# Kernel tuning notes

Hardware: AMD Instinct MI355X
Metric: run time of the kernel (lower is better)

The kernel has to match this reference:

```python
import jax, jax.numpy as jnp
import numpy as np

N_REC_STEPS = 50      # fixed-point iterations for geodesic reconstruction
BN_EPS = 1e-3         # keras BatchNormalization default epsilon


def _dilation2d(x, k):
    # tf.nn.dilation2d, SAME padding: out[p,q] = max_{i,j} x[p+i-1,q+j-1] + k[i,j]
    kk = k[:, :, 0, 0]
    H, W = x.shape[1], x.shape[2]
    xp = jnp.pad(x, ((0, 0), (1, 1), (1, 1), (0, 0)), constant_values=-np.inf)
    vals = [xp[:, i:i + H, j:j + W, :] + kk[i, j] for i in range(3) for j in range(3)]
    return jnp.max(jnp.stack(vals, axis=0), axis=0)


def _erosion2d(x, k):
    # tf.nn.erosion2d (kernel mirrored): out[p,q] = min_{i,j} x[p+i-1,q+j-1] - k[-i,-j]
    kk = k[::-1, ::-1, 0, 0]
    H, W = x.shape[1], x.shape[2]
    xp = jnp.pad(x, ((0, 0), (1, 1), (1, 1), (0, 0)), constant_values=np.inf)
    vals = [xp[:, i:i + H, j:j + W, :] - kk[i, j] for i in range(3) for j in range(3)]
    return jnp.min(jnp.stack(vals, axis=0), axis=0)


def _conv_relu(x, w, b):
    y = jax.lax.conv_general_dilated(x, w, (1, 1), 'VALID',
                                     dimension_numbers=('NHWC', 'HWIO', 'NHWC'))
    return jax.nn.relu(y + b)


def _bn(x, g, b, m, v):
    return g * (x - m) * jax.lax.rsqrt(v + BN_EPS) + b


def _maxpool2(x):
    return jax.lax.reduce_window(x, -np.inf, jax.lax.max,
                                 (1, 2, 2, 1), (1, 2, 2, 1), 'VALID')


def _dilate3_same(x):
    # flat 3x3 structuring element (skimage square(3)) geodesic dilation step
    return jax.lax.reduce_window(x, -np.inf, jax.lax.max,
                                 (1, 3, 3, 1), (1, 1, 1, 1), 'SAME')


def _h_maxima(h, mask):
    # reconstruction-by-dilation of (mask - h) under mask
    marker = mask - h
    def step(m, _):
        m = jnp.minimum(_dilate3_same(m), mask)
        return m, None
    rec, _ = jax.lax.scan(step, marker, None, length=N_REC_STEPS)
    return rec


def setup_inputs() -> dict:
    key = jax.random.key(0)
    ks = jax.random.split(key, 8)
    B, H, W = 32, 256, 256
    inp = {
        'x': jax.random.uniform(ks[0], (B, H, W, 1), dtype=jnp.float32),
        'kernel_open': jnp.zeros((3, 3, 1, 1), jnp.float32),   # flat SE (zero-init)
        'kernel_close': jnp.zeros((3, 3, 1, 1), jnp.float32),
        'conv1_w': 0.1 * jax.random.normal(ks[1], (3, 3, 1, 8), jnp.float32),
        'conv1_b': jnp.zeros((8,), jnp.float32),
        'conv2_w': 0.1 * jax.random.normal(ks[2], (3, 3, 8, 16), jnp.float32),
        'conv2_b': jnp.zeros((16,), jnp.float32),
        'conv3_w': 0.1 * jax.random.normal(ks[3], (3, 3, 16, 32), jnp.float32),
        'conv3_b': jnp.zeros((32,), jnp.float32),
        'conv4_w': 0.1 * jax.random.normal(ks[4], (3, 3, 32, 32), jnp.float32),
        'conv4_b': jnp.zeros((32,), jnp.float32),
        'bn1_g': jnp.ones((8,), jnp.float32), 'bn1_b': jnp.zeros((8,), jnp.float32),
        'bn1_m': jnp.zeros((8,), jnp.float32), 'bn1_v': jnp.ones((8,), jnp.float32),
        'bn2_g': jnp.ones((16,), jnp.float32), 'bn2_b': jnp.zeros((16,), jnp.float32),
        'bn2_m': jnp.zeros((16,), jnp.float32), 'bn2_v': jnp.ones((16,), jnp.float32),
        'bn3_g': jnp.ones((32,), jnp.float32), 'bn3_b': jnp.zeros((32,), jnp.float32),
        'bn3_m': jnp.zeros((32,), jnp.float32), 'bn3_v': jnp.ones((32,), jnp.float32),
        'dense_w': 0.05 * jax.random.uniform(ks[5], (32, 1), dtype=jnp.float32),  # NonNeg
        'dense_b': jnp.zeros((1,), jnp.float32),
    }
    return inp


def reference(x, kernel_open, kernel_close,
              conv1_w, conv1_b, conv2_w, conv2_b, conv3_w, conv3_b, conv4_w, conv4_b,
              bn1_g, bn1_b, bn1_m, bn1_v,
              bn2_g, bn2_b, bn2_m, bn2_v,
              bn3_g, bn3_b, bn3_m, bn3_v,
              dense_w, dense_b):
    # Opening2D then Closing2D (morphological pre-filter)
    xo = _dilation2d(_erosion2d(x, kernel_open), kernel_open)
    xc = _erosion2d(_dilation2d(xo, kernel_close), kernel_close)
    y = _conv_relu(xc, conv1_w, conv1_b)                 # (B,254,254,8)
    y = _bn(y, bn1_g, bn1_b, bn1_m, bn1_v)
    y = _conv_relu(y, conv2_w, conv2_b)                  # (B,252,252,16)
    y = _maxpool2(y)                                     # (B,126,126,16)
    y = _bn(y, bn2_g, bn2_b, bn2_m, bn2_v)
    y = _conv_relu(y, conv3_w, conv3_b)                  # (B,124,124,32)
    y = _bn(y, bn3_g, bn3_b, bn3_m, bn3_v)
    y = _conv_relu(y, conv4_w, conv4_b)                  # (B,122,122,32)
    y = _maxpool2(y)                                     # (B,61,61,32)
    y = jnp.max(y, axis=(1, 2))                          # GlobalMaxPooling2D -> (B,32)
    h = y @ dense_w + dense_b                            # (B,1)
    h = h[:, :, None, None]                              # (B,1,1,1)
    # h-maxima transform: reconstruction by dilation of (xc - h) under xc
    out = _h_maxima(h, xc)                               # (B,256,256,1)
    return (out, h)
```

## Files before the change

kernel.cpp:

```cpp
#include <hip/hip_runtime.h>


#define B_ 32
#define H_ 256
#define W_ 256

__device__ __forceinline__ float4 ld4(const float* p){ return *reinterpret_cast<const float4*>(p); }
__device__ __forceinline__ void st4(float* p, float4 v){ *reinterpret_cast<float4*>(p) = v; }
__device__ __forceinline__ void st4s(float* p, float4 v){ *reinterpret_cast<float4*>(p) = v; }

template<int IS_MAX>
__global__ void morph_k(const float* __restrict__ in, float* __restrict__ out,
                        const float* __restrict__ k9)
{
    int t = blockIdx.x * blockDim.x + threadIdx.x;
    int xq = t & 63; int y = (t >> 6) & 255; int b = t >> 14;
    if (b >= B_) return;
    const float INF = __builtin_inff();
    const float* img = in + (size_t)b * (H_ * W_);
    int x0 = xq * 4;
    float res[4];
    #pragma unroll
    for (int j = 0; j < 4; ++j) res[j] = IS_MAX ? -INF : INF;
    #pragma unroll
    for (int di = -1; di <= 1; ++di) {
        int yy = y + di;
        if (yy < 0 || yy >= H_) continue;
        const float* row = img + yy * W_;
        float w[6];
        w[0] = (x0 > 0) ? row[x0 - 1] : (IS_MAX ? -INF : INF);
        float4 m = ld4(row + x0);
        w[1] = m.x; w[2] = m.y; w[3] = m.z; w[4] = m.w;
        w[5] = (x0 + 4 < W_) ? row[x0 + 4] : (IS_MAX ? -INF : INF);
        #pragma unroll
        for (int dj = -1; dj <= 1; ++dj) {
            float kv = IS_MAX ? k9[(di + 1) * 3 + (dj + 1)]
                              : k9[(1 - di) * 3 + (1 - dj)];
            #pragma unroll
            for (int j = 0; j < 4; ++j) {
                float v = IS_MAX ? (w[j + 1 + dj] + kv) : (w[j + 1 + dj] - kv);
                res[j] = IS_MAX ? fmaxf(res[j], v) : fminf(res[j], v);
            }
        }
    }
    st4(out + (size_t)b * (H_ * W_) + y * W_ + x0,
        make_float4(res[0], res[1], res[2], res[3]));
}

__global__ void conv1_k(const float* __restrict__ xc, float* __restrict__ y1,
                        const float* __restrict__ w, const float* __restrict__ bias,
                        const float* __restrict__ g, const float* __restrict__ bb,
                        const float* __restrict__ mn, const float* __restrict__ vr)
{
    const int S = 254;
    int t = blockIdx.x * blockDim.x + threadIdx.x;
    int total = B_ * S * S;
    if (t >= total) return;
    int x = t % S; int y = (t / S) % S; int b = t / (S * S);
    const float* img = xc + (size_t)b * H_ * W_;
    float acc[8];
    #pragma unroll
    for (int c = 0; c < 8; ++c) acc[c] = bias[c];
    #pragma unroll
    for (int ky = 0; ky < 3; ++ky) {
        #pragma unroll
        for (int kx = 0; kx < 3; ++kx) {
            float iv = img[(y + ky) * W_ + (x + kx)];
            const float* wp = w + (ky * 3 + kx) * 8;
            #pragma unroll
            for (int c = 0; c < 8; ++c) acc[c] = fmaf(iv, wp[c], acc[c]);
        }
    }
    float* op = y1 + (size_t)t * 8;
    #pragma unroll
    for (int c = 0; c < 8; ++c) {
        float z = fmaxf(acc[c], 0.f);
        float s = g[c] / sqrtf(vr[c] + 1.0e-3f);
        op[c] = fmaf(s, z, bb[c] - mn[c] * s);
    }
}

#define C2_PITCH (34 * 34 + 2)
__global__ void __launch_bounds__(256) conv2t_k(
    const float* __restrict__ y1, float* __restrict__ y2,
    const float* __restrict__ w, const float* __restrict__ bias,
    const float* __restrict__ g, const float* __restrict__ bb,
    const float* __restrict__ mn, const float* __restrict__ vr)
{
    const int SIN = 254, POUT = 126;
    __shared__ float lds[8 * C2_PITCH];
    int blk = blockIdx.x;
    int b = blk >> 6; int tt = blk & 63; int ty = tt >> 3, tx = tt & 7;
    int cy0 = ty * 32, cx0 = tx * 32;
    int tid = threadIdx.x;
    const float* in_b = y1 + (size_t)b * SIN * SIN * 8;

    for (int i = tid; i < 34 * 34; i += 256) {
        int r = i / 34, c = i - r * 34;
        int gy = min(cy0 + r, SIN - 1), gx = min(cx0 + c, SIN - 1);
        const float* p = in_b + ((size_t)gy * SIN + gx) * 8;
        float4 a = ld4(p), d = ld4(p + 4);
        lds[0 * C2_PITCH + i] = a.x; lds[1 * C2_PITCH + i] = a.y;
        lds[2 * C2_PITCH + i] = a.z; lds[3 * C2_PITCH + i] = a.w;
        lds[4 * C2_PITCH + i] = d.x; lds[5 * C2_PITCH + i] = d.y;
        lds[6 * C2_PITCH + i] = d.z; lds[7 * C2_PITCH + i] = d.w;
    }
    __syncthreads();

    int lty = tid >> 4, ltx = tid & 15;
    float acc[4][16];
    #pragma unroll
    for (int pos = 0; pos < 4; ++pos)
        #pragma unroll
        for (int c = 0; c < 16; ++c) acc[pos][c] = bias[c];

    #pragma unroll 1
    for (int tap = 0; tap < 9; ++tap) {
        int ky = tap / 3, kx = tap - ky * 3;
        const float* wp = w + tap * 8 * 16;
        #pragma unroll
        for (int pos = 0; pos < 4; ++pos) {
            int pix = (2 * lty + (pos >> 1) + ky) * 34 + (2 * ltx + (pos & 1) + kx);
            float in8[8];
            #pragma unroll
            for (int ci = 0; ci < 8; ++ci) in8[ci] = lds[ci * C2_PITCH + pix];
            #pragma unroll
            for (int ci = 0; ci < 8; ++ci)
                #pragma unroll
                for (int co = 0; co < 16; ++co)
                    acc[pos][co] = fmaf(in8[ci], wp[ci * 16 + co], acc[pos][co]);
        }
    }

    int py = ty * 16 + lty, px = tx * 16 + ltx;
    if (py < POUT && px < POUT) {
        float* op = y2 + ((size_t)b * POUT * POUT + (size_t)py * POUT + px) * 16;
        #pragma unroll
        for (int co = 0; co < 16; ++co) {
            float bst = fmaxf(fmaxf(fmaxf(acc[0][co], 0.f), fmaxf(acc[1][co], 0.f)),
                              fmaxf(fmaxf(acc[2][co], 0.f), fmaxf(acc[3][co], 0.f)));
            float s = g[co] / sqrtf(vr[co] + 1.0e-3f);
            op[co] = fmaf(s, bst, bb[co] - mn[co] * s);
        }
    }
}

template<int CIN, int NCH, int CHP, int SIN>
__device__ __forceinline__ void conv_tile_chunked(
    const float* __restrict__ in_b, const float* __restrict__ w,
    const float* __restrict__ bias, float* lds,
    int y0, int x0, int lty, int ltx, int tid, float acc[32])
{
    const int CHUNK = CIN / NCH, CHQ = CHUNK / 4;
    #pragma unroll
    for (int c = 0; c < 32; ++c) acc[c] = bias[c];
    #pragma unroll 1
    for (int ch = 0; ch < NCH; ++ch) {
        int ci0 = ch * CHUNK;
        if (ch) __syncthreads();
        const int TOT = 18 * 18 * CHQ;
        for (int i = tid; i < TOT; i += 256) {
            int pix = i / CHQ, q = i - pix * CHQ;
            int r = pix / 18, c = pix - r * 18;
            int gy = min(y0 + r, SIN - 1), gx = min(x0 + c, SIN - 1);
            float4 v = ld4(in_b + ((size_t)gy * SIN + gx) * CIN + ci0 + q * 4);
            st4s(lds + (r * 18 + c) * CHP + q * 4, v);
        }
        __syncthreads();
        const float* wb = w + ci0 * 32;
        #pragma unroll 1
        for (int tap = 0; tap < 9; ++tap) {
            int ky = tap / 3, kx = tap - ky * 3;
            const float* lp = lds + ((lty + ky) * 18 + (ltx + kx)) * CHP;
            float v[CHUNK];
            #pragma unroll
            for (int q = 0; q < CHQ; ++q) {
                float4 t4 = *reinterpret_cast<const float4*>(lp + q * 4);
                v[q * 4 + 0] = t4.x; v[q * 4 + 1] = t4.y;
                v[q * 4 + 2] = t4.z; v[q * 4 + 3] = t4.w;
            }
            const float* wt = wb + tap * CIN * 32;
            #pragma unroll
            for (int ci = 0; ci < CHUNK; ++ci)
                #pragma unroll
                for (int co = 0; co < 32; ++co)
                    acc[co] = fmaf(v[ci], wt[ci * 32 + co], acc[co]);
        }
    }
}

__global__ void __launch_bounds__(256) conv3t_k(
    const float* __restrict__ y2, float* __restrict__ y3,
    const float* __restrict__ w, const float* __restrict__ bias,
    const float* __restrict__ g, const float* __restrict__ bb,
    const float* __restrict__ mn, const float* __restrict__ vr)
{
    const int SIN = 126, SOUT = 124;
    __shared__ float lds[18 * 18 * 20];
    int blk = blockIdx.x;
    int b = blk >> 6; int tt = blk & 63; int ty = tt >> 3, tx = tt & 7;
    int tid = threadIdx.x, lty = tid >> 4, ltx = tid & 15;
    float acc[32];
    conv_tile_chunked<16, 1, 20, 126>(y2 + (size_t)b * SIN * SIN * 16, w, bias,
                                      lds, ty * 16, tx * 16, lty, ltx, tid, acc);
    int oy = ty * 16 + lty, ox = tx * 16 + ltx;
    if (oy < SOUT && ox < SOUT) {
        float* op = y3 + ((size_t)b * SOUT * SOUT + (size_t)oy * SOUT + ox) * 32;
        #pragma unroll
        for (int c = 0; c < 32; ++c) {
            float z = fmaxf(acc[c], 0.f);
            float s = g[c] / sqrtf(vr[c] + 1.0e-3f);
            op[c] = fmaf(s, z, bb[c] - mn[c] * s);
        }
    }
}

__global__ void __launch_bounds__(256) conv4t_k(
    const float* __restrict__ y3, float* __restrict__ maxbuf,
    const float* __restrict__ w, const float* __restrict__ bias)
{
    const int SIN = 124, SOUT = 122;
    __shared__ float lds[18 * 18 * 20];
    __shared__ float red[4 * 32];
    int blk = blockIdx.x;
    int b = blk >> 6; int tt = blk & 63; int ty = tt >> 3, tx = tt & 7;
    int tid = threadIdx.x, lty = tid >> 4, ltx = tid & 15;
    float acc[32];
    conv_tile_chunked<32, 2, 20, 124>(y3 + (size_t)b * SIN * SIN * 32, w, bias,
                                      lds, ty * 16, tx * 16, lty, ltx, tid, acc);
    int oy = ty * 16 + lty, ox = tx * 16 + ltx;
    bool valid = (oy < SOUT) && (ox < SOUT);
    #pragma unroll
    for (int c = 0; c < 32; ++c)
        acc[c] = valid ? fmaxf(acc[c], 0.f) : 0.f;
    int lane = tid & 63, wid = tid >> 6;
    #pragma unroll 1
    for (int c = 0; c < 32; ++c) {
        float v = acc[c];
        #pragma unroll
        for (int off = 32; off >= 1; off >>= 1)
            v = fmaxf(v, __shfl_xor(v, off, 64));
        if (lane == 0) red[wid * 32 + c] = v;
    }
    __syncthreads();
    if (tid < 32) {
        int c = tid;
        float mx = fmaxf(fmaxf(red[0 * 32 + c], red[1 * 32 + c]),
                         fmaxf(red[2 * 32 + c], red[3 * 32 + c]));
        atomicMax(reinterpret_cast<int*>(maxbuf) + b * 32 + c, __float_as_int(mx));
    }
}

__global__ void dense_k(const float* __restrict__ maxbuf, const float* __restrict__ dw,
                        const float* __restrict__ db, float* __restrict__ hbuf,
                        float* __restrict__ out_h)
{
    int t = threadIdx.x;
    if (t < B_) {
        float acc = db[0];
        #pragma unroll
        for (int c = 0; c < 32; ++c) acc = fmaf(maxbuf[t * 32 + c], dw[c], acc);
        hbuf[t] = acc;
        out_h[t] = acc;
    }
}

__global__ void minit_k(const float* __restrict__ xc, const float* __restrict__ hbuf,
                        float* __restrict__ m0)
{
    int t = blockIdx.x * blockDim.x + threadIdx.x;
    int b = t >> 14;
    if (b >= B_) return;
    float hv = hbuf[b];
    float4 a = ld4(xc + (size_t)t * 4);
    st4(m0 + (size_t)t * 4, make_float4(a.x - hv, a.y - hv, a.z - hv, a.w - hv));
}

#define FS_R   5
#define FS_IW  80
#define FS_IH  42
__global__ void __launch_bounds__(256) fstep_k(
    const float* __restrict__ msrc, const float* __restrict__ mask,
    float* __restrict__ mdst)
{
    __shared__ float bufA[FS_IH * FS_IW];
    __shared__ float bufB[FS_IH * FS_IW];
    __shared__ float mk[FS_IH * FS_IW];
    const float NINF = -__builtin_inff();

    int blk = blockIdx.x;
    int img = blk >> 5; int tt = blk & 31; int ty = tt >> 2, tx = tt & 3;
    int gy0 = ty * 32 - FS_R;
    int gx0 = tx * 64 - 8;
    int tid = threadIdx.x;
    const float* src_b = msrc + (size_t)img * (H_ * W_);
    const float* msk_b = mask + (size_t)img * (H_ * W_);

    for (int i = tid; i < FS_IH * FS_IW; i += 256) {
        int r = i / FS_IW, c = i - r * FS_IW;
        int gy = gy0 + r, gx = gx0 + c;
        bool in = (gy >= 0) && (gy < H_) && (gx >= 0) && (gx < W_);
        int gidx = gy * W_ + gx;
        bufA[i] = in ? src_b[gidx] : NINF;
        mk[i]   = in ? msk_b[gidx] : NINF;
    }
    __syncthreads();

    float* cur = bufA;
    float* nxt = bufB;
    #pragma unroll 1
    for (int s = 0; s < FS_R; ++s) {
        for (int i = tid; i < FS_IH * (FS_IW / 4); i += 256) {
            int r = i / (FS_IW / 4), q = i - r * (FS_IW / 4);
            int c = q * 4;
            int rm = (r > 0) ? r - 1 : 0, rp = (r < FS_IH - 1) ? r + 1 : FS_IH - 1;
            float h0, h1, h2, h3;
            {
                const float* rw = cur + rm * FS_IW;
                float4 a = *reinterpret_cast<const float4*>(rw + c);
                float L = rw[(c > 0) ? c - 1 : 0];
                float R = rw[(c + 4 < FS_IW) ? c + 4 : FS_IW - 1];
                h0 = fmaxf(fmaxf(L, a.x), a.y);
                h1 = fmaxf(fmaxf(a.x, a.y), a.z);
                h2 = fmaxf(fmaxf(a.y, a.z), a.w);
                h3 = fmaxf(fmaxf(a.z, a.w), R);
            }
            {
                const float* rw = cur + r * FS_IW;
                float4 a = *reinterpret_cast<const float4*>(rw + c);
                float L = rw[(c > 0) ? c - 1 : 0];
                float R = rw[(c + 4 < FS_IW) ? c + 4 : FS_IW - 1];
                h0 = fmaxf(h0, fmaxf(fmaxf(L, a.x), a.y));
                h1 = fmaxf(h1, fmaxf(fmaxf(a.x, a.y), a.z));
                h2 = fmaxf(h2, fmaxf(fmaxf(a.y, a.z), a.w));
                h3 = fmaxf(h3, fmaxf(fmaxf(a.z, a.w), R));
            }
            {
                const float* rw = cur + rp * FS_IW;
                float4 a = *reinterpret_cast<const float4*>(rw + c);
                float L = rw[(c > 0) ? c - 1 : 0];
                float R = rw[(c + 4 < FS_IW) ? c + 4 : FS_IW - 1];
                h0 = fmaxf(h0, fmaxf(fmaxf(L, a.x), a.y));
                h1 = fmaxf(h1, fmaxf(fmaxf(a.x, a.y), a.z));
                h2 = fmaxf(h2, fmaxf(fmaxf(a.y, a.z), a.w));
                h3 = fmaxf(h3, fmaxf(fmaxf(a.z, a.w), R));
            }
            float4 m4 = *reinterpret_cast<const float4*>(mk + r * FS_IW + c);
            float4 o;
            o.x = fminf(h0, m4.x); o.y = fminf(h1, m4.y);
            o.z = fminf(h2, m4.z); o.w = fminf(h3, m4.w);
            *reinterpret_cast<float4*>(nxt + r * FS_IW + c) = o;
        }
        __syncthreads();
        float* tmp = cur; cur = nxt; nxt = tmp;
    }

    float* dst_b = mdst + (size_t)img * (H_ * W_);
    for (int i = tid; i < 32 * 16; i += 256) {
        int r = i >> 4, q = i & 15;
        float4 v = *reinterpret_cast<const float4*>(cur + (FS_R + r) * FS_IW + 8 + q * 4);
        *reinterpret_cast<float4*>(dst_b + (ty * 32 + r) * W_ + tx * 64 + q * 4) = v;
    }
}

extern "C" void kernel_launch(void* const* d_in, const int* in_sizes, int n_in,
                              void* d_out, int out_size, void* d_ws, size_t ws_size,
                              hipStream_t stream) {
    const float* x    = (const float*)d_in[0];
    const float* ko   = (const float*)d_in[1];
    const float* kc   = (const float*)d_in[2];
    const float* c1w  = (const float*)d_in[3];
    const float* c1b  = (const float*)d_in[4];
    const float* c2w  = (const float*)d_in[5];
    const float* c2b  = (const float*)d_in[6];
    const float* c3w  = (const float*)d_in[7];
    const float* c3b  = (const float*)d_in[8];
    const float* c4w  = (const float*)d_in[9];
    const float* c4b  = (const float*)d_in[10];
    const float* bn1g = (const float*)d_in[11];
    const float* bn1b = (const float*)d_in[12];
    const float* bn1m = (const float*)d_in[13];
    const float* bn1v = (const float*)d_in[14];
    const float* bn2g = (const float*)d_in[15];
    const float* bn2b = (const float*)d_in[16];
    const float* bn2m = (const float*)d_in[17];
    const float* bn2v = (const float*)d_in[18];
    const float* bn3g = (const float*)d_in[19];
    const float* bn3b = (const float*)d_in[20];
    const float* bn3m = (const float*)d_in[21];
    const float* bn3v = (const float*)d_in[22];
    const float* dw   = (const float*)d_in[23];
    const float* db   = (const float*)d_in[24];
    float* out = (float*)d_out;
    float* ws  = (float*)d_ws;

    float* xc     = ws;
    float* A      = ws + 2097152;
    float* Bbuf   = ws + 18613248;
    float* maxbuf = ws + 26741760;
    float* hbuf   = ws + 26742784;
    float* t0 = A;
    float* t1 = A + 2097152;

    const int NQ_BLOCKS = (B_ * H_ * W_ / 4) / 256;

    morph_k<0><<<NQ_BLOCKS, 256, 0, stream>>>(x,  t0, ko);
    morph_k<1><<<NQ_BLOCKS, 256, 0, stream>>>(t0, t1, ko);
    morph_k<1><<<NQ_BLOCKS, 256, 0, stream>>>(t1, t0, kc);
    morph_k<0><<<NQ_BLOCKS, 256, 0, stream>>>(t0, xc, kc);

    conv1_k<<<(B_ * 254 * 254 + 255) / 256, 256, 0, stream>>>(xc, A, c1w, c1b,
                                                              bn1g, bn1b, bn1m, bn1v);
    conv2t_k<<<B_ * 64, 256, 0, stream>>>(A, Bbuf, c2w, c2b, bn2g, bn2b, bn2m, bn2v);
    conv3t_k<<<B_ * 64, 256, 0, stream>>>(Bbuf, A, c3w, c3b, bn3g, bn3b, bn3m, bn3v);
    hipMemsetAsync(maxbuf, 0, 32 * 32 * sizeof(float), stream);
    conv4t_k<<<B_ * 64, 256, 0, stream>>>(A, maxbuf, c4w, c4b);
    dense_k<<<1, 64, 0, stream>>>(maxbuf, dw, db, hbuf, out + B_ * H_ * W_);

    minit_k<<<NQ_BLOCKS, 256, 0, stream>>>(xc, hbuf, t0);
    for (int j = 0; j < 10; ++j) {
        const float* src = (j & 1) ? t1 : t0;
        float* dst = (j == 9) ? out : ((j & 1) ? t0 : t1);
        fstep_k<<<B_ * 32, 256, 0, stream>>>(src, xc, dst);
    }
}
```

Before: 573.6 us.

## Fuse four morphology passes into one LDS-tiled kernel; chunk conv channels to cut LDS

Replaces the four separate erosion/dilation launches with one kernel that loads a 4-pixel-haloed tile into shared memory and applies all four 3x3 ops in place. Out-of-image cells are reset to each next op's identity value. This removes three full-image global round trips and three launches, at the cost of redundant halo work. Separately, conv2/3/4 now stage input channels in smaller chunks, reducing LDS per block to raise occupancy, but this adds extra syncs and reloads.

```diff
diff --git a/kernel.cpp b/kernel.cpp
--- a/kernel.cpp
+++ b/kernel.cpp
@@ -9,42 +9,92 @@
 __device__ __forceinline__ void st4(float* p, float4 v){ *reinterpret_cast<float4*>(p) = v; }
 __device__ __forceinline__ void st4s(float* p, float4 v){ *reinterpret_cast<float4*>(p) = v; }
 
+#define MF_W 72
+#define MF_H 40
 template<int IS_MAX>
-__global__ void morph_k(const float* __restrict__ in, float* __restrict__ out,
-                        const float* __restrict__ k9)
-{
-    int t = blockIdx.x * blockDim.x + threadIdx.x;
-    int xq = t & 63; int y = (t >> 6) & 255; int b = t >> 14;
-    if (b >= B_) return;
+__device__ __forceinline__ void morph_op(
+    const float* __restrict__ cur, float* __restrict__ nxt,
+    const float* __restrict__ k9, float ident_next,
+    int gy0, int gx0, int tid)
+{
+    float kv[3][3];
+    #pragma unroll
+    for (int di = -1; di <= 1; ++di)
+        #pragma unroll
+        for (int dj = -1; dj <= 1; ++dj)
+            kv[di + 1][dj + 1] = IS_MAX ? k9[(di + 1) * 3 + (dj + 1)]
+                                        : k9[(1 - di) * 3 + (1 - dj)];
     const float INF = __builtin_inff();
-    const float* img = in + (size_t)b * (H_ * W_);
-    int x0 = xq * 4;
-    float res[4];
-    #pragma unroll
-    for (int j = 0; j < 4; ++j) res[j] = IS_MAX ? -INF : INF;
-    #pragma unroll
-    for (int di = -1; di <= 1; ++di) {
-        int yy = y + di;
-        if (yy < 0 || yy >= H_) continue;
-        const float* row = img + yy * W_;
-        float w[6];
-        w[0] = (x0 > 0) ? row[x0 - 1] : (IS_MAX ? -INF : INF);
-        float4 m = ld4(row + x0);
-        w[1] = m.x; w[2] = m.y; w[3] = m.z; w[4] = m.w;
-        w[5] = (x0 + 4 < W_) ? row[x0 + 4] : (IS_MAX ? -INF : INF);
-        #pragma unroll
-        for (int dj = -1; dj <= 1; ++dj) {
-            float kv = IS_MAX ? k9[(di + 1) * 3 + (dj + 1)]
-                              : k9[(1 - di) * 3 + (1 - dj)];
+    for (int i = tid; i < MF_H * (MF_W / 4); i += 256) {
+        int r = i / (MF_W / 4), q = i - r * (MF_W / 4);
+        int c = q * 4;
+        float res[4];
+        #pragma unroll
+        for (int j = 0; j < 4; ++j) res[j] = IS_MAX ? -INF : INF;
+        #pragma unroll
+        for (int di = -1; di <= 1; ++di) {
+            int rr = min(max(r + di, 0), MF_H - 1);
+            const float* rw = cur + rr * MF_W;
+            float w[6];
+            w[0] = rw[(c > 0) ? c - 1 : 0];
+            float4 a = *reinterpret_cast<const float4*>(rw + c);
+            w[1] = a.x; w[2] = a.y; w[3] = a.z; w[4] = a.w;
+            w[5] = rw[(c + 4 < MF_W) ? c + 4 : MF_W - 1];
             #pragma unroll
-            for (int j = 0; j < 4; ++j) {
-                float v = IS_MAX ? (w[j + 1 + dj] + kv) : (w[j + 1 + dj] - kv);
-                res[j] = IS_MAX ? fmaxf(res[j], v) : fminf(res[j], v);
-            }
-        }
-    }
-    st4(out + (size_t)b * (H_ * W_) + y * W_ + x0,
-        make_float4(res[0], res[1], res[2], res[3]));
+            for (int dj = -1; dj <= 1; ++dj) {
+                float k = kv[di + 1][dj + 1];
+                #pragma unroll
+                for (int j = 0; j < 4; ++j) {
+                    float v = IS_MAX ? (w[j + 1 + dj] + k) : (w[j + 1 + dj] - k);
+                    res[j] = IS_MAX ? fmaxf(res[j], v) : fminf(res[j], v);
+                }
+            }
+        }
+        int gy = gy0 + r;
+        #pragma unroll
+        for (int j = 0; j < 4; ++j) {
+            int gx = gx0 + c + j;
+            bool in = (gy >= 0) && (gy < H_) && (gx >= 0) && (gx < W_);
+            res[j] = in ? res[j] : ident_next;
+        }
+        *reinterpret_cast<float4*>(nxt + r * MF_W + c) =
+            make_float4(res[0], res[1], res[2], res[3]);
+    }
+}
+
+__global__ void __launch_bounds__(256) morphf_k(
+    const float* __restrict__ x, float* __restrict__ xc,
+    const float* __restrict__ ko, const float* __restrict__ kc)
+{
+    __shared__ float bufA[MF_H * MF_W];
+    __shared__ float bufB[MF_H * MF_W];
+    int blk = blockIdx.x;
+    int img = blk >> 5; int tt = blk & 31; int ty = tt >> 2, tx = tt & 3;
+    int gy0 = ty * 32 - 4, gx0 = tx * 64 - 4;
+    int tid = threadIdx.x;
+    const float* src = x + (size_t)img * (H_ * W_);
+    const float INF = __builtin_inff();
+    for (int i = tid; i < MF_H * MF_W; i += 256) {
+        int r = i / MF_W, c = i - r * MF_W;
+        int gy = gy0 + r, gx = gx0 + c;
+        bool in = (gy >= 0) && (gy < H_) && (gx >= 0) && (gx < W_);
+        bufA[i] = in ? src[gy * W_ + gx] : INF;
+    }
+    __syncthreads();
+    morph_op<0>(bufA, bufB, ko, -INF, gy0, gx0, tid);
+    __syncthreads();
+    morph_op<1>(bufB, bufA, ko, -INF, gy0, gx0, tid);
+    __syncthreads();
+    morph_op<1>(bufA, bufB, kc,  INF, gy0, gx0, tid);
+    __syncthreads();
+    morph_op<0>(bufB, bufA, kc,  0.f, gy0, gx0, tid);
+    __syncthreads();
+    float* dst = xc + (size_t)img * (H_ * W_);
+    for (int i = tid; i < 32 * 16; i += 256) {
+        int r = i >> 4, q = i & 15;
+        float4 v = *reinterpret_cast<const float4*>(bufA + (4 + r) * MF_W + 4 + q * 4);
+        *reinterpret_cast<float4*>(dst + (ty * 32 + r) * W_ + tx * 64 + q * 4) = v;
+    }
 }
 
 __global__ void conv1_k(const float* __restrict__ xc, float* __restrict__ y1,
@@ -88,26 +138,14 @@
     const float* __restrict__ mn, const float* __restrict__ vr)
 {
     const int SIN = 254, POUT = 126;
-    __shared__ float lds[8 * C2_PITCH];
+    __shared__ float lds[4 * C2_PITCH];
     int blk = blockIdx.x;
     int b = blk >> 6; int tt = blk & 63; int ty = tt >> 3, tx = tt & 7;
     int cy0 = ty * 32, cx0 = tx * 32;
     int tid = threadIdx.x;
+    int lty = tid >> 4, ltx = tid & 15;
     const float* in_b = y1 + (size_t)b * SIN * SIN * 8;
 
-    for (int i = tid; i < 34 * 34; i += 256) {
-        int r = i / 34, c = i - r * 34;
-        int gy = min(cy0 + r, SIN - 1), gx = min(cx0 + c, SIN - 1);
-        const float* p = in_b + ((size_t)gy * SIN + gx) * 8;
-        float4 a = ld4(p), d = ld4(p + 4);
-        lds[0 * C2_PITCH + i] = a.x; lds[1 * C2_PITCH + i] = a.y;
-        lds[2 * C2_PITCH + i] = a.z; lds[3 * C2_PITCH + i] = a.w;
-        lds[4 * C2_PITCH + i] = d.x; lds[5 * C2_PITCH + i] = d.y;
-        lds[6 * C2_PITCH + i] = d.z; lds[7 * C2_PITCH + i] = d.w;
-    }
-    __syncthreads();
-
-    int lty = tid >> 4, ltx = tid & 15;
     float acc[4][16];
     #pragma unroll
     for (int pos = 0; pos < 4; ++pos)
@@ -115,20 +153,33 @@
         for (int c = 0; c < 16; ++c) acc[pos][c] = bias[c];
 
     #pragma unroll 1
-    for (int tap = 0; tap < 9; ++tap) {
-        int ky = tap / 3, kx = tap - ky * 3;
-        const float* wp = w + tap * 8 * 16;
-        #pragma unroll
-        for (int pos = 0; pos < 4; ++pos) {
-            int pix = (2 * lty + (pos >> 1) + ky) * 34 + (2 * ltx + (pos & 1) + kx);
-            float in8[8];
+    for (int ch = 0; ch < 2; ++ch) {
+        int ci0 = ch * 4;
+        if (ch) __syncthreads();
+        for (int i = tid; i < 34 * 34; i += 256) {
+            int r = i / 34, c = i - r * 34;
+            int gy = min(cy0 + r, SIN - 1), gx = min(cx0 + c, SIN - 1);
+            float4 a = ld4(in_b + ((size_t)gy * SIN + gx) * 8 + ci0);
+            lds[0 * C2_PITCH + i] = a.x; lds[1 * C2_PITCH + i] = a.y;
+            lds[2 * C2_PITCH + i] = a.z; lds[3 * C2_PITCH + i] = a.w;
+        }
+        __syncthreads();
+        #pragma unroll 1
+        for (int tap = 0; tap < 9; ++tap) {
+            int ky = tap / 3, kx = tap - ky * 3;
+            const float* wp = w + (tap * 8 + ci0) * 16;
             #pragma unroll
-            for (int ci = 0; ci < 8; ++ci) in8[ci] = lds[ci * C2_PITCH + pix];
-            #pragma unroll
-            for (int ci = 0; ci < 8; ++ci)
+            for (int pos = 0; pos < 4; ++pos) {
+                int pix = (2 * lty + (pos >> 1) + ky) * 34 + (2 * ltx + (pos & 1) + kx);
+                float in4[4];
                 #pragma unroll
-                for (int co = 0; co < 16; ++co)
-                    acc[pos][co] = fmaf(in8[ci], wp[ci * 16 + co], acc[pos][co]);
+                for (int ci = 0; ci < 4; ++ci) in4[ci] = lds[ci * C2_PITCH + pix];
+                #pragma unroll
+                for (int ci = 0; ci < 4; ++ci)
+                    #pragma unroll
+                    for (int co = 0; co < 16; ++co)
+                        acc[pos][co] = fmaf(in4[ci], wp[ci * 16 + co], acc[pos][co]);
+            }
         }
     }
 
@@ -196,12 +247,12 @@
     const float* __restrict__ mn, const float* __restrict__ vr)
 {
     const int SIN = 126, SOUT = 124;
-    __shared__ float lds[18 * 18 * 20];
+    __shared__ float lds[18 * 18 * 12];
     int blk = blockIdx.x;
     int b = blk >> 6; int tt = blk & 63; int ty = tt >> 3, tx = tt & 7;
     int tid = threadIdx.x, lty = tid >> 4, ltx = tid & 15;
     float acc[32];
-    conv_tile_chunked<16, 1, 20, 126>(y2 + (size_t)b * SIN * SIN * 16, w, bias,
+    conv_tile_chunked<16, 2, 12, 126>(y2 + (size_t)b * SIN * SIN * 16, w, bias,
                                       lds, ty * 16, tx * 16, lty, ltx, tid, acc);
     int oy = ty * 16 + lty, ox = tx * 16 + ltx;
     if (oy < SOUT && ox < SOUT) {
@@ -220,13 +271,13 @@
     const float* __restrict__ w, const float* __restrict__ bias)
 {
     const int SIN = 124, SOUT = 122;
-    __shared__ float lds[18 * 18 * 20];
+    __shared__ float lds[18 * 18 * 12];
     __shared__ float red[4 * 32];
     int blk = blockIdx.x;
     int b = blk >> 6; int tt = blk & 63; int ty = tt >> 3, tx = tt & 7;
     int tid = threadIdx.x, lty = tid >> 4, ltx = tid & 15;
     float acc[32];
-    conv_tile_chunked<32, 2, 20, 124>(y3 + (size_t)b * SIN * SIN * 32, w, bias,
+    conv_tile_chunked<32, 4, 12, 124>(y3 + (size_t)b * SIN * SIN * 32, w, bias,
                                       lds, ty * 16, tx * 16, lty, ltx, tid, acc);
     int oy = ty * 16 + lty, ox = tx * 16 + ltx;
     bool valid = (oy < SOUT) && (ox < SOUT);
@@ -404,10 +455,7 @@
 
     const int NQ_BLOCKS = (B_ * H_ * W_ / 4) / 256;
 
-    morph_k<0><<<NQ_BLOCKS, 256, 0, stream>>>(x,  t0, ko);
-    morph_k<1><<<NQ_BLOCKS, 256, 0, stream>>>(t0, t1, ko);
-    morph_k<1><<<NQ_BLOCKS, 256, 0, stream>>>(t1, t0, kc);
-    morph_k<0><<<NQ_BLOCKS, 256, 0, stream>>>(t0, xc, kc);
+    morphf_k<<<B_ * 32, 256, 0, stream>>>(x, xc, ko, kc);
 
     conv1_k<<<(B_ * 254 * 254 + 255) / 256, 256, 0, stream>>>(xc, A, c1w, c1b,
                                                               bn1g, bn1b, bn1m, bn1v);
```

Result: no change. 579.5 us (+1.0%).
